# Kernel tuning notes

Measured on AMD Instinct MI355X. Metric: run time of the kernel, lower is better.

## Reference

```python
import jax, jax.numpy as jnp
import numpy as np

N, D, H, C = 100000, 128, 8, 16  # nodes, units=H*C, heads, per-head channels
E = 400000                        # edges per edge set (2 edge sets)
LN_EPS = 1e-3                     # keras LayerNormalization default epsilon


def setup_inputs() -> dict:
    key = jax.random.key(0)
    ks = jax.random.split(key, 16)
    def dense(k, i, o):
        return jax.random.normal(k, (i, o), jnp.float32) / np.float32(np.sqrt(i))
    return dict(
        x=jax.random.normal(ks[0], (N, D), jnp.float32),
        src0=jax.random.randint(ks[1], (E,), 0, N),
        dst0=jax.random.randint(ks[2], (E,), 0, N),
        src1=jax.random.randint(ks[3], (E,), 0, N),
        dst1=jax.random.randint(ks[4], (E,), 0, N),
        Wk=dense(ks[5], D, D), bk=jnp.zeros((D,), jnp.float32),
        Wm=dense(ks[6], D, D), bm=jnp.zeros((D,), jnp.float32),
        Wq=dense(ks[7], D, D), bq=jnp.zeros((D,), jnp.float32),
        Wa=dense(ks[8], D, D), ba=jnp.zeros((D,), jnp.float32),
        Watt0=jax.random.normal(ks[9], (H, C, C), jnp.float32) / np.float32(np.sqrt(C)),
        Wmsg0=jax.random.normal(ks[10], (H, C, C), jnp.float32) / np.float32(np.sqrt(C)),
        Watt1=jax.random.normal(ks[11], (H, C, C), jnp.float32) / np.float32(np.sqrt(C)),
        Wmsg1=jax.random.normal(ks[12], (H, C, C), jnp.float32) / np.float32(np.sqrt(C)),
        prior0=jnp.ones((H,), jnp.float32),
        prior1=jnp.ones((H,), jnp.float32),
        skip=jnp.ones((), jnp.float32),
        gamma=jnp.ones((D,), jnp.float32),
        beta=jnp.zeros((D,), jnp.float32),
    )


def reference(x, src0, dst0, src1, dst1, Wk, bk, Wm, bm, Wq, bq, Wa, ba,
              Watt0, Wmsg0, Watt1, Wmsg1, prior0, prior1, skip, gamma, beta):
    # Node-level projections, split per head: [N, H, C]
    k = (x @ Wk + bk).reshape(N, H, C)
    m = (x @ Wm + bm).reshape(N, H, C)
    q = (x @ Wq + bq).reshape(N, H, C)
    scale = 1.0 / jnp.sqrt(jnp.float32(C))

    def edge_terms(src, dst, Watt, Wmsg, prior):
        # per-edge-type relation projections of gathered sender keys/messages
        ke = jnp.einsum('ehk,hkl->ehl', k[src], Watt)          # [E, H, C]
        score = jnp.einsum('ehl,ehl->eh', ke, q[dst]) * prior * scale  # [E, H]
        msg = jnp.einsum('ehk,hkl->ehl', m[src], Wmsg)          # [E, H, C]
        return score, msg

    s0, m0 = edge_terms(src0, dst0, Watt0, Wmsg0, prior0)
    s1, m1 = edge_terms(src1, dst1, Watt1, Wmsg1, prior1)

    # Joint segment softmax over all incoming edges (both edge sets) per receiver
    scores = jnp.concatenate([s0, s1], axis=0)   # [2E, H]
    msgs = jnp.concatenate([m0, m1], axis=0)     # [2E, H, C]
    recv = jnp.concatenate([dst0, dst1], axis=0)

    smax = jax.ops.segment_max(scores, recv, num_segments=N)   # [N, H]
    ex = jnp.exp(scores - smax[recv])
    denom = jax.ops.segment_sum(ex, recv, num_segments=N)      # [N, H]
    d_e = denom[recv]
    attn = ex / jnp.where(d_e > 0, d_e, 1.0)                   # [2E, H]

    pooled = jax.ops.segment_sum(attn[:, :, None] * msgs, recv,
                                 num_segments=N).reshape(N, D)  # [N, D]

    # aggr(gelu(pooled)); weighted skip; layer norm
    h = jax.nn.gelu(pooled, approximate=False) @ Wa + ba
    alpha = jax.nn.sigmoid(skip)
    out = alpha * h + (1.0 - alpha) * x
    mu = jnp.mean(out, axis=-1, keepdims=True)
    var = jnp.var(out, axis=-1, keepdims=True)
    out = (out - mu) * jax.lax.rsqrt(var + LN_EPS) * gamma + beta
    return out
```

## Files before the change

### kernel.cpp

```cpp
#include <hip/hip_runtime.h>
#include <hip/hip_bf16.h>
#include <math.h>

#define N_NODES 100000
#define DIM 128
#define NH 8
#define NC 16
#define E_EDGES 400000
#define LN_EPS 1e-3f
#define SCAN_B 1024
#define PROJ_GRID 512

typedef __attribute__((ext_vector_type(8))) short short8v;
typedef __attribute__((ext_vector_type(4))) short short4v;
typedef __attribute__((ext_vector_type(4))) float float4v;

__device__ __forceinline__ short bf16bits(float v) {
    __hip_bfloat16 b = __float2bfloat16(v);
    return *(short*)&b;
}

__device__ __forceinline__ void bf2x2(unsigned v, float& a, float& b) {
    a = __uint_as_float(v << 16);
    b = __uint_as_float(v & 0xffff0000u);
}

__global__ __launch_bounds__(128) void fuse_weights(
    const float* __restrict__ Wk, const float* __restrict__ bk,
    const float* __restrict__ Wm, const float* __restrict__ bm,
    const float* __restrict__ Wq, const float* __restrict__ bq,
    const float* __restrict__ Wa, const float* __restrict__ ba,
    const float* __restrict__ Watt0, const float* __restrict__ Wmsg0,
    const float* __restrict__ Watt1, const float* __restrict__ Wmsg1,
    const float* __restrict__ prior0, const float* __restrict__ prior1,
    __hip_bfloat16* __restrict__ Wt, float* __restrict__ bias)
{
    const int c = blockIdx.x;
    const int d = threadIdx.x;
    const int sec = c >> 7, j = c & 127, h = j >> 4, l = j & 15;
    float v, b;
    if (sec == 4)      { v = Wq[d * DIM + j]; b = bq[j]; }
    else if (sec == 5) { v = Wa[d * DIM + j]; b = ba[j]; }
    else {
        const float* W1 = (sec < 2) ? Wk : Wm;
        const float* bs = (sec < 2) ? bk : bm;
        const float* W2 = (sec == 0) ? Watt0 : (sec == 1) ? Watt1
                          : (sec == 2) ? Wmsg0 : Wmsg1;
        float scale = (sec == 0) ? prior0[h] * 0.25f
                    : (sec == 1) ? prior1[h] * 0.25f : 1.f;
        float s = 0.f, sb = 0.f;
        #pragma unroll
        for (int kk = 0; kk < NC; ++kk) {
            float w2 = W2[h * 256 + kk * 16 + l];
            s  = fmaf(W1[d * DIM + h * 16 + kk], w2, s);
            sb = fmaf(bs[h * 16 + kk], w2, sb);
        }
        v = s * scale; b = sb * scale;
    }
    Wt[(size_t)c * DIM + d] = __float2bfloat16(v);
    if (d == 0) bias[c] = b;
}

__global__ __launch_bounds__(512) void proj_mfma(
    const float* __restrict__ x,
    const __hip_bfloat16* __restrict__ Wt,
    const float* __restrict__ bias,
    __hip_bfloat16* __restrict__ km,
    __hip_bfloat16* __restrict__ qb)
{
    __shared__ __align__(16) short xs[2][32 * DIM];
    const int tid = threadIdx.x;
    const int wave = tid >> 6, lane = tid & 63;
    const int quad = lane >> 4, mcol = lane & 15;
    const int nt = N_NODES / 32;

    short8v wf[5][4];
    float4v bv[5];
    #pragma unroll
    for (int s = 0; s < 5; ++s) {
        const int c0 = s * 128 + wave * 16;
        const short* wp = (const short*)Wt + (size_t)(c0 + mcol) * DIM + quad * 8;
        #pragma unroll
        for (int kb = 0; kb < 4; ++kb)
            wf[s][kb] = *(const short8v*)(wp + kb * 32);
        bv[s] = *(const float4v*)(bias + c0 + quad * 4);
    }

    const int srow = tid >> 4, sc8 = tid & 15;
    const int swz = ((sc8 ^ (srow & 7)) * 8);

    int t = blockIdx.x;
    if (t >= nt) return;

    float4v f0 = *(const float4v*)(x + (size_t)(t * 32 + srow) * DIM + sc8 * 8);
    float4v f1 = *(const float4v*)(x + (size_t)(t * 32 + srow) * DIM + sc8 * 8 + 4);
    {
        short8v sv;
        #pragma unroll
        for (int j = 0; j < 4; ++j) { sv[j] = bf16bits(f0[j]); sv[j + 4] = bf16bits(f1[j]); }
        *(short8v*)(xs[0] + srow * DIM + swz) = sv;
    }
    {
        int nn = t + PROJ_GRID;
        if (nn < nt) {
            f0 = *(const float4v*)(x + (size_t)(nn * 32 + srow) * DIM + sc8 * 8);
            f1 = *(const float4v*)(x + (size_t)(nn * 32 + srow) * DIM + sc8 * 8 + 4);
        }
    }

    int cur = 0;
    for (; t < nt; t += PROJ_GRID) {
        __syncthreads();

        short8v b0[4], b1[4];
        #pragma unroll
        for (int kb = 0; kb < 4; ++kb) {
            const int ch = ((quad + kb * 4) ^ (mcol & 7)) * 8;
            b0[kb] = *(const short8v*)(xs[cur] + mcol * DIM + ch);
            b1[kb] = *(const short8v*)(xs[cur] + (mcol + 16) * DIM + ch);
        }

        const int r0 = t * 32;

        #pragma unroll
        for (int e = 0; e < 2; ++e) {
            float4v aK0 = {0.f,0.f,0.f,0.f}, aK1 = {0.f,0.f,0.f,0.f};
            float4v aM0 = {0.f,0.f,0.f,0.f}, aM1 = {0.f,0.f,0.f,0.f};
            #pragma unroll
            for (int kb = 0; kb < 4; ++kb) {
                aK0 = __builtin_amdgcn_mfma_f32_16x16x32_bf16(wf[e][kb],     b0[kb], aK0, 0, 0, 0);
                aK1 = __builtin_amdgcn_mfma_f32_16x16x32_bf16(wf[e][kb],     b1[kb], aK1, 0, 0, 0);
                aM0 = __builtin_amdgcn_mfma_f32_16x16x32_bf16(wf[2 + e][kb], b0[kb], aM0, 0, 0, 0);
                aM1 = __builtin_amdgcn_mfma_f32_16x16x32_bf16(wf[2 + e][kb], b1[kb], aM1, 0, 0, 0);
            }
            short8v o0, o1;
            #pragma unroll
            for (int g = 0; g < 4; ++g) {
                o0[g]     = bf16bits(aK0[g] + bv[e][g]);
                o0[g + 4] = bf16bits(aM0[g] + bv[2 + e][g]);
                o1[g]     = bf16bits(aK1[g] + bv[e][g]);
                o1[g + 4] = bf16bits(aM1[g] + bv[2 + e][g]);
            }
            short* dp = (short*)km
                      + ((size_t)(r0 + mcol) + (size_t)e * N_NODES) * 256
                      + (wave * 4 + quad) * 8;
            *(short8v*)dp              = o0;
            *(short8v*)(dp + 16 * 256) = o1;
        }

        {
            float4v a0v = {0.f,0.f,0.f,0.f}, a1v = {0.f,0.f,0.f,0.f};
            #pragma unroll
            for (int kb = 0; kb < 4; ++kb) {
                a0v = __builtin_amdgcn_mfma_f32_16x16x32_bf16(wf[4][kb], b0[kb], a0v, 0, 0, 0);
                a1v = __builtin_amdgcn_mfma_f32_16x16x32_bf16(wf[4][kb], b1[kb], a1v, 0, 0, 0);
            }
            short4v o0, o1;
            #pragma unroll
            for (int g = 0; g < 4; ++g) {
                o0[g] = bf16bits(a0v[g] + bv[4][g]);
                o1[g] = bf16bits(a1v[g] + bv[4][g]);
            }
            short* dp = (short*)qb + (size_t)(r0 + mcol) * DIM + wave * 16 + quad * 4;
            *(short4v*)dp              = o0;
            *(short4v*)(dp + 16 * DIM) = o1;
        }

        int nn = t + PROJ_GRID;
        if (nn < nt) {
            short8v sv;
            #pragma unroll
            for (int j = 0; j < 4; ++j) { sv[j] = bf16bits(f0[j]); sv[j + 4] = bf16bits(f1[j]); }
            *(short8v*)(xs[cur ^ 1] + srow * DIM + swz) = sv;
            int n2 = nn + PROJ_GRID;
            if (n2 < nt) {
                f0 = *(const float4v*)(x + (size_t)(n2 * 32 + srow) * DIM + sc8 * 8);
                f1 = *(const float4v*)(x + (size_t)(n2 * 32 + srow) * DIM + sc8 * 8 + 4);
            }
        }
        cur ^= 1;
    }
}

__global__ __launch_bounds__(256) void hist_kernel(
    const int* __restrict__ dst0, const int* __restrict__ dst1,
    int* __restrict__ counts)
{
    int e = blockIdx.x * 256 + threadIdx.x;
    if (e < E_EDGES) atomicAdd(&counts[dst0[e]], 1);
    int e1 = e - E_EDGES;
    if (e1 >= 0 && e1 < E_EDGES) atomicAdd(&counts[dst1[e1]], 1);
}

__global__ __launch_bounds__(SCAN_B) void scanA_kernel(
    const int* __restrict__ counts, int* __restrict__ row_ptr,
    int* __restrict__ bsum)
{
    __shared__ int buf[2][SCAN_B];
    int i = blockIdx.x * SCAN_B + threadIdx.x;
    int v = (i < N_NODES) ? counts[i] : 0;
    int cur = 0;
    buf[0][threadIdx.x] = v;
    __syncthreads();
    #pragma unroll
    for (int off = 1; off < SCAN_B; off <<= 1) {
        int t = buf[cur][threadIdx.x];
        int add = (threadIdx.x >= off) ? buf[cur][threadIdx.x - off] : 0;
        buf[cur ^ 1][threadIdx.x] = t + add;
        cur ^= 1;
        __syncthreads();
    }
    int inc = buf[cur][threadIdx.x];
    if (i < N_NODES) row_ptr[i] = inc - v;
    if (threadIdx.x == SCAN_B - 1) bsum[blockIdx.x] = inc;
}

__global__ __launch_bounds__(128) void scanB_kernel(int* __restrict__ bsum, int nblocks)
{
    __shared__ int buf[2][128];
    int t = threadIdx.x;
    int v = (t < nblocks) ? bsum[t] : 0;
    buf[0][t] = v;
    __syncthreads();
    int cur = 0;
    #pragma unroll
    for (int off = 1; off < 128; off <<= 1) {
        int a = buf[cur][t];
        if (t >= off) a += buf[cur][t - off];
        buf[cur ^ 1][t] = a;
        cur ^= 1;
        __syncthreads();
    }
    if (t < nblocks) bsum[t] = buf[cur][t] - v;
}

__global__ __launch_bounds__(SCAN_B) void scanC_kernel(
    int* __restrict__ row_ptr, int* __restrict__ cursor,
    const int* __restrict__ bsum)
{
    int i = blockIdx.x * SCAN_B + threadIdx.x;
    if (i < N_NODES) {
        int r = row_ptr[i] + bsum[blockIdx.x];
        row_ptr[i] = r;
        cursor[i] = r;
    }
}

__global__ __launch_bounds__(256) void scatter_kernel(
    const int* __restrict__ src0, const int* __restrict__ dst0,
    const int* __restrict__ src1, const int* __restrict__ dst1,
    int* __restrict__ cursor, unsigned int* __restrict__ eidx)
{
    int e = blockIdx.x * 256 + threadIdx.x;
    if (e < E_EDGES) {
        int d = dst0[e];
        int pos = atomicAdd(&cursor[d], 1);
        eidx[pos] = (unsigned int)src0[e];
    }
    int e1 = e - E_EDGES;
    if (e1 >= 0 && e1 < E_EDGES) {
        int d = dst1[e1];
        int pos = atomicAdd(&cursor[d], 1);
        eidx[pos] = (unsigned int)(src1[e1] + N_NODES);
    }
}

__global__ __launch_bounds__(256) void agg_kernel(
    const char* __restrict__ km,
    const uint2* __restrict__ qv,
    const int* __restrict__ row_ptr, const int* __restrict__ counts,
    const unsigned int* __restrict__ eidx,
    uint2* __restrict__ pooled)
{
    const int wave = threadIdx.x >> 6, lane = threadIdx.x & 63;
    const int n = blockIdx.x * 4 + wave;
    if (n >= N_NODES) return;
    const int start = row_ptr[n], cnt = counts[n];
    const int hi = lane >> 5;
    const int glane = lane & 31;
    const unsigned g16 = (unsigned)glane << 4;

    uint2 qu = qv[(size_t)n * 32 + glane];
    float q0, q1, q2, q3;
    bf2x2(qu.x, q0, q1); bf2x2(qu.y, q2, q3);

    float a0 = 0.f, a1 = 0.f, a2 = 0.f, a3 = 0.f, den = 0.f;

#define PAIR_ACC(u)                                                          \
    {                                                                        \
        float k0, k1, k2, k3, m0, m1, m2, m3;                                \
        bf2x2((u).x, k0, k1); bf2x2((u).y, k2, k3);                          \
        bf2x2((u).z, m0, m1); bf2x2((u).w, m2, m3);                          \
        float p = fmaf(k3, q3, fmaf(k2, q2, fmaf(k1, q1, k0 * q0)));         \
        p += __shfl_xor(p, 1, 64);                                           \
        p += __shfl_xor(p, 2, 64);                                           \
        float e = __expf(p);                                                 \
        den += e;                                                            \
        a0 = fmaf(e, m0, a0); a1 = fmaf(e, m1, a1);                          \
        a2 = fmaf(e, m2, a2); a3 = fmaf(e, m3, a3);                          \
    }

    int i = 0;
    for (; i + 8 <= cnt; i += 8) {
        unsigned ra = eidx[start + i + hi];
        unsigned rb = eidx[start + i + 2 + hi];
        unsigned rc = eidx[start + i + 4 + hi];
        unsigned rd = eidx[start + i + 6 + hi];
        uint4 ua = *(const uint4*)(km + (((size_t)ra << 9) | g16));
        uint4 ub = *(const uint4*)(km + (((size_t)rb << 9) | g16));
        uint4 uc = *(const uint4*)(km + (((size_t)rc << 9) | g16));
        uint4 ud = *(const uint4*)(km + (((size_t)rd << 9) | g16));
        PAIR_ACC(ua); PAIR_ACC(ub); PAIR_ACC(uc); PAIR_ACC(ud);
    }
    for (; i + 2 <= cnt; i += 2) {
        unsigned ra = eidx[start + i + hi];
        uint4 ua = *(const uint4*)(km + (((size_t)ra << 9) | g16));
        PAIR_ACC(ua);
    }
    if (i < cnt) {
        unsigned ra = eidx[start + i];
        uint4 ua = *(const uint4*)(km + (((size_t)ra << 9) | g16));
        float k0, k1, k2, k3, m0, m1, m2, m3;
        bf2x2(ua.x, k0, k1); bf2x2(ua.y, k2, k3);
        bf2x2(ua.z, m0, m1); bf2x2(ua.w, m2, m3);
        float p = fmaf(k3, q3, fmaf(k2, q2, fmaf(k1, q1, k0 * q0)));
        p += __shfl_xor(p, 1, 64);
        p += __shfl_xor(p, 2, 64);
        float e = hi ? 0.f : __expf(p);
        den += e;
        a0 = fmaf(e, m0, a0); a1 = fmaf(e, m1, a1);
        a2 = fmaf(e, m2, a2); a3 = fmaf(e, m3, a3);
    }
#undef PAIR_ACC

    den += __shfl_xor(den, 32, 64);
    a0 += __shfl_xor(a0, 32, 64);
    a1 += __shfl_xor(a1, 32, 64);
    a2 += __shfl_xor(a2, 32, 64);
    a3 += __shfl_xor(a3, 32, 64);

    float inv = (den > 0.f) ? (1.f / den) : 0.f;
    float v0 = a0 * inv, v1 = a1 * inv, v2 = a2 * inv, v3 = a3 * inv;

    float s0 = hi ? v2 : v0;
    float s1 = hi ? v3 : v1;
    s0 = 0.5f * s0 * (1.f + erff(s0 * 0.70710678118654752f));
    s1 = 0.5f * s1 * (1.f + erff(s1 * 0.70710678118654752f));
    unsigned pk = ((unsigned)(unsigned short)bf16bits(s0))
                | ((unsigned)(unsigned short)bf16bits(s1) << 16);
    unsigned ph = __shfl_xor(pk, 32, 64);
    if (!hi) {
        uint2 o; o.x = pk; o.y = ph;
        pooled[(size_t)n * 32 + glane] = o;
    }
}

__global__ __launch_bounds__(256) void final_mfma(
    const __hip_bfloat16* __restrict__ pooled,
    const __hip_bfloat16* __restrict__ Wt,
    const float* __restrict__ bias,
    const float* __restrict__ x,
    const float* __restrict__ skip, const float* __restrict__ gamma,
    const float* __restrict__ beta, float* __restrict__ out)
{
    __shared__ float hs[32][DIM];
    const int wave = threadIdx.x >> 6, lane = threadIdx.x & 63;
    const int quad = lane >> 4, mcol = lane & 15;
    const int r0 = blockIdx.x * 32;

    short8v a0[4], a1[4];
    const short* pp0 = (const short*)pooled + (size_t)(r0 + mcol) * DIM + quad * 8;
    const short* pp1 = pp0 + 16 * DIM;
    #pragma unroll
    for (int kb = 0; kb < 4; ++kb) {
        a0[kb] = *(const short8v*)(pp0 + kb * 32);
        a1[kb] = *(const short8v*)(pp1 + kb * 32);
    }
    const float alpha = 1.f / (1.f + expf(-skip[0]));

    #pragma unroll
    for (int t = 0; t < 2; ++t) {
        const int c0 = wave * 32 + t * 16;
        const short* wp = (const short*)Wt + (size_t)(640 + c0 + mcol) * DIM + quad * 8;
        float4v acc0 = {0.f, 0.f, 0.f, 0.f};
        float4v acc1 = {0.f, 0.f, 0.f, 0.f};
        #pragma unroll
        for (int kb = 0; kb < 4; ++kb) {
            short8v bfr = *(const short8v*)(wp + kb * 32);
            acc0 = __builtin_amdgcn_mfma_f32_16x16x32_bf16(a0[kb], bfr, acc0, 0, 0, 0);
            acc1 = __builtin_amdgcn_mfma_f32_16x16x32_bf16(a1[kb], bfr, acc1, 0, 0, 0);
        }
        const float bcol = bias[640 + c0 + mcol];
        const int cc = c0 + mcol;
        const int rq = quad * 4;
        #pragma unroll
        for (int g = 0; g < 4; ++g) {
            int rA = rq + g, rB = rq + 16 + g;
            hs[rA][cc] = alpha * (acc0[g] + bcol)
                       + (1.f - alpha) * x[(size_t)(r0 + rA) * DIM + cc];
            hs[rB][cc] = alpha * (acc1[g] + bcol)
                       + (1.f - alpha) * x[(size_t)(r0 + rB) * DIM + cc];
        }
    }
    __syncthreads();

    float gam0 = gamma[lane], gam1 = gamma[lane + 64];
    float bet0 = beta[lane],  bet1 = beta[lane + 64];
    for (int r = wave; r < 32; r += 4) {
        int row = r0 + r;
        float v0 = hs[r][lane], v1 = hs[r][lane + 64];
        float s = v0 + v1, s2 = v0 * v0 + v1 * v1;
        #pragma unroll
        for (int off = 1; off < 64; off <<= 1) {
            s  += __shfl_xor(s,  off, 64);
            s2 += __shfl_xor(s2, off, 64);
        }
        float mu = s * (1.f / 128.f);
        float var = s2 * (1.f / 128.f) - mu * mu;
        float rstd = rsqrtf(var + LN_EPS);
        out[(size_t)row * DIM + lane]      = (v0 - mu) * rstd * gam0 + bet0;
        out[(size_t)row * DIM + lane + 64] = (v1 - mu) * rstd * gam1 + bet1;
    }
}

extern "C" void kernel_launch(void* const* d_in, const int* in_sizes, int n_in,
                              void* d_out, int out_size, void* d_ws, size_t ws_size,
                              hipStream_t stream) {
    const float* x     = (const float*)d_in[0];
    const int*   src0  = (const int*)d_in[1];
    const int*   dst0  = (const int*)d_in[2];
    const int*   src1  = (const int*)d_in[3];
    const int*   dst1  = (const int*)d_in[4];
    const float* Wk    = (const float*)d_in[5];
    const float* bk    = (const float*)d_in[6];
    const float* Wm    = (const float*)d_in[7];
    const float* bm    = (const float*)d_in[8];
    const float* Wq    = (const float*)d_in[9];
    const float* bq    = (const float*)d_in[10];
    const float* Wa    = (const float*)d_in[11];
    const float* ba    = (const float*)d_in[12];
    const float* Watt0 = (const float*)d_in[13];
    const float* Wmsg0 = (const float*)d_in[14];
    const float* Watt1 = (const float*)d_in[15];
    const float* Wmsg1 = (const float*)d_in[16];
    const float* prior0= (const float*)d_in[17];
    const float* prior1= (const float*)d_in[18];
    const float* skip  = (const float*)d_in[19];
    const float* gamma = (const float*)d_in[20];
    const float* beta  = (const float*)d_in[21];
    float* out = (float*)d_out;

    const size_t nd = (size_t)N_NODES * DIM;
    char* wsb = (char*)d_ws;
    __hip_bfloat16* Wt    = (__hip_bfloat16*)wsb;  wsb += (size_t)768 * DIM * 2;
    float* bias           = (float*)wsb;           wsb += 768 * 4;
    __hip_bfloat16* km    = (__hip_bfloat16*)wsb;  wsb += (size_t)2 * N_NODES * 256 * 2;
    __hip_bfloat16* qb    = (__hip_bfloat16*)wsb;  wsb += nd * 2;
    __hip_bfloat16* pooled= (__hip_bfloat16*)wsb;  wsb += nd * 2;
    int* counts  = (int*)wsb;                      wsb += (size_t)N_NODES * 4;
    int* row_ptr = (int*)wsb;                      wsb += (size_t)N_NODES * 4;
    int* cursor  = (int*)wsb;                      wsb += (size_t)N_NODES * 4;
    int* bsum    = (int*)wsb;                      wsb += 128 * 4;
    unsigned int* eidx = (unsigned int*)wsb;

    hipMemsetAsync(counts, 0, (size_t)N_NODES * 4, stream);

    const int scan_blocks = (N_NODES + SCAN_B - 1) / SCAN_B;
    const int edge_blocks = (2 * E_EDGES + 255) / 256;

    hist_kernel<<<dim3(edge_blocks), dim3(256), 0, stream>>>(dst0, dst1, counts);
    scanA_kernel<<<dim3(scan_blocks), dim3(SCAN_B), 0, stream>>>(counts, row_ptr, bsum);
    scanB_kernel<<<dim3(1), dim3(128), 0, stream>>>(bsum, scan_blocks);
    scanC_kernel<<<dim3(scan_blocks), dim3(SCAN_B), 0, stream>>>(row_ptr, cursor, bsum);
    scatter_kernel<<<dim3(edge_blocks), dim3(256), 0, stream>>>(
        src0, dst0, src1, dst1, cursor, eidx);

    fuse_weights<<<dim3(768), dim3(128), 0, stream>>>(
        Wk, bk, Wm, bm, Wq, bq, Wa, ba,
        Watt0, Wmsg0, Watt1, Wmsg1, prior0, prior1, Wt, bias);
    proj_mfma<<<dim3(PROJ_GRID), dim3(512), 0, stream>>>(
        x, Wt, bias, km, qb);

    agg_kernel<<<dim3((N_NODES + 3) / 4), dim3(256), 0, stream>>>(
        (const char*)km, (const uint2*)qb, row_ptr, counts, eidx,
        (uint2*)pooled);

    final_mfma<<<dim3(N_NODES / 32), dim3(256), 0, stream>>>(
        pooled, Wt, bias, x, skip, gamma, beta, out);
}
```

Baseline: 358.6 us.

## Split fused key/message gather into separate score and weighted-sum kernels

```diff
diff --git a/kernel.cpp b/kernel.cpp
--- a/kernel.cpp
+++ b/kernel.cpp
@@ -65,7 +65,8 @@
     const float* __restrict__ x,
     const __hip_bfloat16* __restrict__ Wt,
     const float* __restrict__ bias,
-    __hip_bfloat16* __restrict__ km,
+    __hip_bfloat16* __restrict__ ka,
+    __hip_bfloat16* __restrict__ mg,
     __hip_bfloat16* __restrict__ qb)
 {
     __shared__ __align__(16) short xs[2][32 * DIM];
@@ -121,47 +122,28 @@
         }
 
         const int r0 = t * 32;
-
-        #pragma unroll
-        for (int e = 0; e < 2; ++e) {
-            float4v aK0 = {0.f,0.f,0.f,0.f}, aK1 = {0.f,0.f,0.f,0.f};
-            float4v aM0 = {0.f,0.f,0.f,0.f}, aM1 = {0.f,0.f,0.f,0.f};
+        #pragma unroll
+        for (int s = 0; s < 5; ++s) {
+            float4v acc0 = {0.f, 0.f, 0.f, 0.f};
+            float4v acc1 = {0.f, 0.f, 0.f, 0.f};
             #pragma unroll
             for (int kb = 0; kb < 4; ++kb) {
-                aK0 = __builtin_amdgcn_mfma_f32_16x16x32_bf16(wf[e][kb],     b0[kb], aK0, 0, 0, 0);
-                aK1 = __builtin_amdgcn_mfma_f32_16x16x32_bf16(wf[e][kb],     b1[kb], aK1, 0, 0, 0);
-                aM0 = __builtin_amdgcn_mfma_f32_16x16x32_bf16(wf[2 + e][kb], b0[kb], aM0, 0, 0, 0);
-                aM1 = __builtin_amdgcn_mfma_f32_16x16x32_bf16(wf[2 + e][kb], b1[kb], aM1, 0, 0, 0);
+                acc0 = __builtin_amdgcn_mfma_f32_16x16x32_bf16(wf[s][kb], b0[kb], acc0, 0, 0, 0);
+                acc1 = __builtin_amdgcn_mfma_f32_16x16x32_bf16(wf[s][kb], b1[kb], acc1, 0, 0, 0);
             }
-            short8v o0, o1;
-            #pragma unroll
-            for (int g = 0; g < 4; ++g) {
-                o0[g]     = bf16bits(aK0[g] + bv[e][g]);
-                o0[g + 4] = bf16bits(aM0[g] + bv[2 + e][g]);
-                o1[g]     = bf16bits(aK1[g] + bv[e][g]);
-                o1[g + 4] = bf16bits(aM1[g] + bv[2 + e][g]);
-            }
-            short* dp = (short*)km
-                      + ((size_t)(r0 + mcol) + (size_t)e * N_NODES) * 256
-                      + (wave * 4 + quad) * 8;
-            *(short8v*)dp              = o0;
-            *(short8v*)(dp + 16 * 256) = o1;
-        }
-
-        {
-            float4v a0v = {0.f,0.f,0.f,0.f}, a1v = {0.f,0.f,0.f,0.f};
-            #pragma unroll
-            for (int kb = 0; kb < 4; ++kb) {
-                a0v = __builtin_amdgcn_mfma_f32_16x16x32_bf16(wf[4][kb], b0[kb], a0v, 0, 0, 0);
-                a1v = __builtin_amdgcn_mfma_f32_16x16x32_bf16(wf[4][kb], b1[kb], a1v, 0, 0, 0);
-            }
+            __hip_bfloat16* dst =
+                (s == 0) ? ka :
+                (s == 1) ? ka + (size_t)N_NODES * DIM :
+                (s == 2) ? mg :
+                (s == 3) ? mg + (size_t)N_NODES * DIM :
+                           qb;
+            short* dp = (short*)dst + (size_t)(r0 + mcol) * DIM + wave * 16 + quad * 4;
             short4v o0, o1;
             #pragma unroll
             for (int g = 0; g < 4; ++g) {
-                o0[g] = bf16bits(a0v[g] + bv[4][g]);
-                o1[g] = bf16bits(a1v[g] + bv[4][g]);
+                o0[g] = bf16bits(acc0[g] + bv[s][g]);
+                o1[g] = bf16bits(acc1[g] + bv[s][g]);
             }
-            short* dp = (short*)qb + (size_t)(r0 + mcol) * DIM + wave * 16 + quad * 4;
             *(short4v*)dp              = o0;
             *(short4v*)(dp + 16 * DIM) = o1;
         }
@@ -265,12 +247,13 @@
     }
 }
 
-__global__ __launch_bounds__(256) void agg_kernel(
-    const char* __restrict__ km,
+__global__ __launch_bounds__(256) void score_kernel(
+    const char* __restrict__ ka,
     const uint2* __restrict__ qv,
     const int* __restrict__ row_ptr, const int* __restrict__ counts,
     const unsigned int* __restrict__ eidx,
-    uint2* __restrict__ pooled)
+    __hip_bfloat16* __restrict__ w,
+    float* __restrict__ invden)
 {
     const int wave = threadIdx.x >> 6, lane = threadIdx.x & 63;
     const int n = blockIdx.x * 4 + wave;
@@ -278,26 +261,26 @@
     const int start = row_ptr[n], cnt = counts[n];
     const int hi = lane >> 5;
     const int glane = lane & 31;
-    const unsigned g16 = (unsigned)glane << 4;
+    const unsigned g8 = (unsigned)glane << 3;
+    const int head = glane >> 2;
+    const bool wlane = ((glane & 3) == 0);
 
     uint2 qu = qv[(size_t)n * 32 + glane];
     float q0, q1, q2, q3;
     bf2x2(qu.x, q0, q1); bf2x2(qu.y, q2, q3);
 
-    float a0 = 0.f, a1 = 0.f, a2 = 0.f, a3 = 0.f, den = 0.f;
-
-#define PAIR_ACC(u)                                                          \
+    float den = 0.f;
+
+#define SC_CONS(u, pos)                                                      \
     {                                                                        \
-        float k0, k1, k2, k3, m0, m1, m2, m3;                                \
+        float k0, k1, k2, k3;                                                \
         bf2x2((u).x, k0, k1); bf2x2((u).y, k2, k3);                          \
-        bf2x2((u).z, m0, m1); bf2x2((u).w, m2, m3);                          \
         float p = fmaf(k3, q3, fmaf(k2, q2, fmaf(k1, q1, k0 * q0)));         \
         p += __shfl_xor(p, 1, 64);                                           \
         p += __shfl_xor(p, 2, 64);                                           \
         float e = __expf(p);                                                 \
         den += e;                                                            \
-        a0 = fmaf(e, m0, a0); a1 = fmaf(e, m1, a1);                          \
-        a2 = fmaf(e, m2, a2); a3 = fmaf(e, m3, a3);                          \
+        if (wlane) w[(size_t)(pos) * 8 + head] = __float2bfloat16(e);        \
     }
 
     int i = 0;
@@ -306,40 +289,105 @@
         unsigned rb = eidx[start + i + 2 + hi];
         unsigned rc = eidx[start + i + 4 + hi];
         unsigned rd = eidx[start + i + 6 + hi];
-        uint4 ua = *(const uint4*)(km + (((size_t)ra << 9) | g16));
-        uint4 ub = *(const uint4*)(km + (((size_t)rb << 9) | g16));
-        uint4 uc = *(const uint4*)(km + (((size_t)rc << 9) | g16));
-        uint4 ud = *(const uint4*)(km + (((size_t)rd << 9) | g16));
-        PAIR_ACC(ua); PAIR_ACC(ub); PAIR_ACC(uc); PAIR_ACC(ud);
+        uint2 ua = *(const uint2*)(ka + (((size_t)ra << 8) | g8));
+        uint2 ub = *(const uint2*)(ka + (((size_t)rb << 8) | g8));
+        uint2 uc = *(const uint2*)(ka + (((size_t)rc << 8) | g8));
+        uint2 ud = *(const uint2*)(ka + (((size_t)rd << 8) | g8));
+        SC_CONS(ua, start + i + hi);
+        SC_CONS(ub, start + i + 2 + hi);
+        SC_CONS(uc, start + i + 4 + hi);
+        SC_CONS(ud, start + i + 6 + hi);
     }
     for (; i + 2 <= cnt; i += 2) {
         unsigned ra = eidx[start + i + hi];
-        uint4 ua = *(const uint4*)(km + (((size_t)ra << 9) | g16));
-        PAIR_ACC(ua);
+        uint2 ua = *(const uint2*)(ka + (((size_t)ra << 8) | g8));
+        SC_CONS(ua, start + i + hi);
     }
     if (i < cnt) {
         unsigned ra = eidx[start + i];
-        uint4 ua = *(const uint4*)(km + (((size_t)ra << 9) | g16));
-        float k0, k1, k2, k3, m0, m1, m2, m3;
+        uint2 ua = *(const uint2*)(ka + (((size_t)ra << 8) | g8));
+        float k0, k1, k2, k3;
         bf2x2(ua.x, k0, k1); bf2x2(ua.y, k2, k3);
-        bf2x2(ua.z, m0, m1); bf2x2(ua.w, m2, m3);
         float p = fmaf(k3, q3, fmaf(k2, q2, fmaf(k1, q1, k0 * q0)));
         p += __shfl_xor(p, 1, 64);
         p += __shfl_xor(p, 2, 64);
         float e = hi ? 0.f : __expf(p);
         den += e;
-        a0 = fmaf(e, m0, a0); a1 = fmaf(e, m1, a1);
-        a2 = fmaf(e, m2, a2); a3 = fmaf(e, m3, a3);
-    }
-#undef PAIR_ACC
+        if (wlane && !hi) w[(size_t)(start + i) * 8 + head] = __float2bfloat16(e);
+    }
+#undef SC_CONS
 
     den += __shfl_xor(den, 32, 64);
+    if (!hi && wlane) {
+        float inv = (den > 0.f) ? (1.f / den) : 0.f;
+        invden[(size_t)n * 8 + head] = inv;
+    }
+}
+
+__global__ __launch_bounds__(256) void sum_kernel(
+    const char* __restrict__ mg,
+    const __hip_bfloat16* __restrict__ w,
+    const float* __restrict__ invden,
+    const int* __restrict__ row_ptr, const int* __restrict__ counts,
+    const unsigned int* __restrict__ eidx,
+    uint2* __restrict__ pooled)
+{
+    const int wave = threadIdx.x >> 6, lane = threadIdx.x & 63;
+    const int n = blockIdx.x * 4 + wave;
+    if (n >= N_NODES) return;
+    const int start = row_ptr[n], cnt = counts[n];
+    const int hi = lane >> 5;
+    const int glane = lane & 31;
+    const unsigned g8 = (unsigned)glane << 3;
+    const int head = glane >> 2;
+
+    float a0 = 0.f, a1 = 0.f, a2 = 0.f, a3 = 0.f;
+
+#define SM_CONS(u, wv_)                                                      \
+    {                                                                        \
+        float m0, m1, m2, m3;                                                \
+        bf2x2((u).x, m0, m1); bf2x2((u).y, m2, m3);                          \
+        a0 = fmaf(wv_, m0, a0); a1 = fmaf(wv_, m1, a1);                      \
+        a2 = fmaf(wv_, m2, a2); a3 = fmaf(wv_, m3, a3);                      \
+    }
+
+    int i = 0;
+    for (; i + 8 <= cnt; i += 8) {
+        unsigned ra = eidx[start + i + hi];
+        unsigned rb = eidx[start + i + 2 + hi];
+        unsigned rc = eidx[start + i + 4 + hi];
+        unsigned rd = eidx[start + i + 6 + hi];
+        uint2 ua = *(const uint2*)(mg + (((size_t)ra << 8) | g8));
+        uint2 ub = *(const uint2*)(mg + (((size_t)rb << 8) | g8));
+        uint2 uc = *(const uint2*)(mg + (((size_t)rc << 8) | g8));
+        uint2 ud = *(const uint2*)(mg + (((size_t)rd << 8) | g8));
+        float wa = __bfloat162float(w[(size_t)(start + i + hi) * 8 + head]);
+        float wb = __bfloat162float(w[(size_t)(start + i + 2 + hi) * 8 + head]);
+        float wc = __bfloat162float(w[(size_t)(start + i + 4 + hi) * 8 + head]);
+        float wd = __bfloat162float(w[(size_t)(start + i + 6 + hi) * 8 + head]);
+        SM_CONS(ua, wa); SM_CONS(ub, wb); SM_CONS(uc, wc); SM_CONS(ud, wd);
+    }
+    for (; i + 2 <= cnt; i += 2) {
+        unsigned ra = eidx[start + i + hi];
+        uint2 ua = *(const uint2*)(mg + (((size_t)ra << 8) | g8));
+        float wa = __bfloat162float(w[(size_t)(start + i + hi) * 8 + head]);
+        SM_CONS(ua, wa);
+    }
+    if (i < cnt) {
+        unsigned ra = eidx[start + i];
+        uint2 ua = *(const uint2*)(mg + (((size_t)ra << 8) | g8));
+        float wa = hi ? 0.f
+                      : __bfloat162float(w[(size_t)(start + i) * 8 + head]);
+        SM_CONS(ua, wa);
+    }
+#undef SM_CONS
+
     a0 += __shfl_xor(a0, 32, 64);
     a1 += __shfl_xor(a1, 32, 64);
     a2 += __shfl_xor(a2, 32, 64);
     a3 += __shfl_xor(a3, 32, 64);
 
-    float inv = (den > 0.f) ? (1.f / den) : 0.f;
+    const float inv = invden[(size_t)n * 8 + head];
     float v0 = a0 * inv, v1 = a1 * inv, v2 = a2 * inv, v3 = a3 * inv;
 
     float s0 = hi ? v2 : v0;
@@ -454,14 +502,17 @@
     char* wsb = (char*)d_ws;
     __hip_bfloat16* Wt    = (__hip_bfloat16*)wsb;  wsb += (size_t)768 * DIM * 2;
     float* bias           = (float*)wsb;           wsb += 768 * 4;
-    __hip_bfloat16* km    = (__hip_bfloat16*)wsb;  wsb += (size_t)2 * N_NODES * 256 * 2;
+    __hip_bfloat16* ka    = (__hip_bfloat16*)wsb;  wsb += 2 * nd * 2;
+    __hip_bfloat16* mg    = (__hip_bfloat16*)wsb;  wsb += 2 * nd * 2;
     __hip_bfloat16* qb    = (__hip_bfloat16*)wsb;  wsb += nd * 2;
-    __hip_bfloat16* pooled= (__hip_bfloat16*)wsb;  wsb += nd * 2;
+    __hip_bfloat16* w     = (__hip_bfloat16*)wsb;  wsb += (size_t)2 * E_EDGES * 8 * 2;
+    float* invden         = (float*)wsb;           wsb += (size_t)N_NODES * 8 * 4;
     int* counts  = (int*)wsb;                      wsb += (size_t)N_NODES * 4;
     int* row_ptr = (int*)wsb;                      wsb += (size_t)N_NODES * 4;
     int* cursor  = (int*)wsb;                      wsb += (size_t)N_NODES * 4;
     int* bsum    = (int*)wsb;                      wsb += 128 * 4;
     unsigned int* eidx = (unsigned int*)wsb;
+    __hip_bfloat16* pooled = ka;
 
     hipMemsetAsync(counts, 0, (size_t)N_NODES * 4, stream);
 
@@ -479,11 +530,12 @@
         Wk, bk, Wm, bm, Wq, bq, Wa, ba,
         Watt0, Wmsg0, Watt1, Wmsg1, prior0, prior1, Wt, bias);
     proj_mfma<<<dim3(PROJ_GRID), dim3(512), 0, stream>>>(
-        x, Wt, bias, km, qb);
-
-    agg_kernel<<<dim3((N_NODES + 3) / 4), dim3(256), 0, stream>>>(
-        (const char*)km, (const uint2*)qb, row_ptr, counts, eidx,
-        (uint2*)pooled);
+        x, Wt, bias, ka, mg, qb);
+
+    score_kernel<<<dim3((N_NODES + 3) / 4), dim3(256), 0, stream>>>(
+        (const char*)ka, (const uint2*)qb, row_ptr, counts, eidx, w, invden);
+    sum_kernel<<<dim3((N_NODES + 3) / 4), dim3(256), 0, stream>>>(
+        (const char*)mg, w, invden, row_ptr, counts, eidx, (uint2*)pooled);
 
     final_mfma<<<dim3(N_NODES / 32), dim3(256), 0, stream>>>(
         pooled, Wt, bias, x, skip, gamma, beta, out);
```

Result: slower. 401.9 us (+12.1%).
